# Kernel optimization log

Measured on AMD Instinct MI355X. Metric: run time of the kernel, lower is better.

The kernel has to match this reference:

```python
import jax, jax.numpy as jnp
import numpy as np
import math

D_MODEL = 1024
N_HEADS = 16
D_FF = 4096
KERNEL = 25
EPS = 1e-5


def setup_inputs() -> dict:
    key = jax.random.key(0)
    ks = jax.random.split(key, 16)
    B, L, D = 2, 2048, D_MODEL
    s = 0.02
    inp = {
        'x': jax.random.normal(ks[0], (B, L, D), dtype=jnp.float32),
        'Wq': jax.random.normal(ks[1], (D, D), dtype=jnp.float32) * s,
        'bq': jnp.zeros((D,), jnp.float32),
        'Wk': jax.random.normal(ks[2], (D, D), dtype=jnp.float32) * s,
        'bk': jnp.zeros((D,), jnp.float32),
        'Wv': jax.random.normal(ks[3], (D, D), dtype=jnp.float32) * s,
        'bv': jnp.zeros((D,), jnp.float32),
        'Wo': jax.random.normal(ks[4], (D, D), dtype=jnp.float32) * s,
        'bo': jnp.zeros((D,), jnp.float32),
        'W1': jax.random.normal(ks[5], (D_FF, D), dtype=jnp.float32) * s,
        'b1': jnp.zeros((D_FF,), jnp.float32),
        'W2': jax.random.normal(ks[6], (D, D_FF), dtype=jnp.float32) * s,
        'b2': jnp.zeros((D,), jnp.float32),
        'g1': jnp.ones((D,), jnp.float32),
        'be1': jnp.zeros((D,), jnp.float32),
        'g2': jnp.ones((D,), jnp.float32),
        'be2': jnp.zeros((D,), jnp.float32),
    }
    return inp


def moving_avg(x):
    # torch AvgPool1d(kernel=25, stride=1, padding=12, count_include_pad=True)
    # x: (B, L, D) -> trend: (B, L, D)
    pad = KERNEL // 2
    xp = jnp.pad(x, ((0, 0), (pad, pad), (0, 0)))
    c = jnp.cumsum(xp, axis=1)
    c = jnp.concatenate([jnp.zeros_like(c[:, :1]), c], axis=1)
    return (c[:, KERNEL:] - c[:, :-KERNEL]) / KERNEL


def layernorm(x, g, b):
    mu = jnp.mean(x, axis=-1, keepdims=True)
    var = jnp.mean((x - mu) ** 2, axis=-1, keepdims=True)
    return (x - mu) * jax.lax.rsqrt(var + EPS) * g + b


def reference(x, Wq, bq, Wk, bk, Wv, bv, Wo, bo, W1, b1, W2, b2, g1, be1, g2, be2):
    B, L, D = x.shape
    H, dk = N_HEADS, D // N_HEADS
    # projections (torch Linear: y = x @ W.T + b)
    q = (x @ Wq.T + bq).reshape(B, L, H, dk).transpose(0, 2, 1, 3)
    k = (x @ Wk.T + bk).reshape(B, L, H, dk).transpose(0, 2, 1, 3)
    v = (x @ Wv.T + bv).reshape(B, L, H, dk).transpose(0, 2, 1, 3)
    scores = jnp.einsum('bhld,bhmd->bhlm', q, k) / math.sqrt(dk)
    t = jnp.arange(L, dtype=jnp.float32)
    time_bias = -0.1 * jnp.abs(t[None, :] - t[:, None])  # (L, L)
    attn = jax.nn.softmax(scores + time_bias[None, None], axis=-1)
    ao = jnp.einsum('bhlm,bhmd->bhld', attn, v)
    ao = ao.transpose(0, 2, 1, 3).reshape(B, L, D)
    attn_out = ao @ Wo.T + bo
    x = x + attn_out
    x = moving_avg(x)  # trend kept (x, _ = decomp1(x))
    x = layernorm(x, g1, be1)
    ff = jax.nn.gelu(x @ W1.T + b1, approximate=False) @ W2.T + b2
    x = x + ff
    x = moving_avg(x)  # trend kept again
    x = layernorm(x, g2, be2)
    return x
```

## Files before the change

### kernel.cpp

```cpp
#include <hip/hip_runtime.h>
#include <hip/hip_bf16.h>
#include <math.h>

#define DMODEL 1024
#define LSEQ   2048
#define BATCH  2
#define NHEADS 16
#define DHEAD  64
#define DFF    4096
#define MROWS  (BATCH*LSEQ)

typedef __attribute__((ext_vector_type(8))) short short8;
typedef __attribute__((ext_vector_type(4))) float f32x4;
using bf16 = __hip_bfloat16;

static __device__ __forceinline__ f32x4 mfma16(short8 a, short8 b, f32x4 c) {
    return __builtin_amdgcn_mfma_f32_16x16x32_bf16(a, b, c, 0, 0, 0);
}

static __device__ __forceinline__ void gload16(const void* g, void* l) {
    __builtin_amdgcn_global_load_lds(
        (const __attribute__((address_space(1))) char*)g,
        (__attribute__((address_space(3))) char*)l, 16, 0, 0);
}

static __device__ __forceinline__ bf16 b16(float v) { return __float2bfloat16(v); }
static __device__ __forceinline__ float f32(bf16 v) { return __bfloat162float(v); }

__global__ void f2b_all(const float* __restrict__ x, const float* __restrict__ W1,
                        const float* __restrict__ W2,
                        const float* Wq, const float* Wk, const float* Wv, const float* Wo,
                        const float* bq, const float* bk, const float* bv,
                        bf16* __restrict__ xb, bf16* __restrict__ W1b, bf16* __restrict__ W2b,
                        bf16* __restrict__ Wqkvb, bf16* __restrict__ Wob,
                        float* __restrict__ bqkv) {
    int i = blockIdx.x * blockDim.x + threadIdx.x;
    const float* in; bf16* out;
    switch (blockIdx.y) {
        case 0: in = x;  out = xb;  break;
        case 1: in = W1; out = W1b; break;
        case 2: in = W2; out = W2b; break;
        case 3: {
            const int w = i >> 18, r = i & ((1 << 18) - 1);
            const float* ws4[4] = {Wq, Wk, Wv, Wo};
            bf16* os4[4] = {Wqkvb, Wqkvb + (DMODEL * DMODEL), Wqkvb + 2 * (DMODEL * DMODEL), Wob};
            float4 v = reinterpret_cast<const float4*>(ws4[w])[r];
            union { ushort4 u; bf16 h[4]; } o;
            o.h[0] = b16(v.x); o.h[1] = b16(v.y); o.h[2] = b16(v.z); o.h[3] = b16(v.w);
            reinterpret_cast<ushort4*>(os4[w])[r] = o.u;
            return;
        }
        default:
            if (i < DMODEL / 4) {
                reinterpret_cast<float4*>(bqkv)[i]                  = reinterpret_cast<const float4*>(bq)[i];
                reinterpret_cast<float4*>(bqkv)[DMODEL / 4 + i]     = reinterpret_cast<const float4*>(bk)[i];
                reinterpret_cast<float4*>(bqkv)[2 * DMODEL / 4 + i] = reinterpret_cast<const float4*>(bv)[i];
            }
            return;
    }
    float4 v = reinterpret_cast<const float4*>(in)[i];
    union { ushort4 u; bf16 h[4]; } o;
    o.h[0] = b16(v.x); o.h[1] = b16(v.y); o.h[2] = b16(v.z); o.h[3] = b16(v.w);
    reinterpret_cast<ushort4*>(out)[i] = o.u;
}

template<int S, bool RESB16>
__global__ __launch_bounds__(256) void reduce_kernel(const void* __restrict__ resv,
                                                     const bf16* __restrict__ P,
                                                     const float* __restrict__ bias,
                                                     bf16* __restrict__ outb, int n4) {
    int i = blockIdx.x * blockDim.x + threadIdx.x;
    if (i >= n4) return;
    float4 acc;
    if (RESB16) {
        union { ushort4 u; bf16 h[4]; } r;
        r.u = reinterpret_cast<const ushort4*>(resv)[i];
        acc.x = f32(r.h[0]); acc.y = f32(r.h[1]); acc.z = f32(r.h[2]); acc.w = f32(r.h[3]);
    } else {
        acc = reinterpret_cast<const float4*>(resv)[i];
    }
#pragma unroll
    for (int s = 0; s < S; ++s) {
        union { ushort4 u; bf16 h[4]; } p;
        p.u = reinterpret_cast<const ushort4*>(P)[i + (size_t)s * (MROWS * DMODEL / 4)];
        acc.x += f32(p.h[0]); acc.y += f32(p.h[1]);
        acc.z += f32(p.h[2]); acc.w += f32(p.h[3]);
    }
    float4 bs = reinterpret_cast<const float4*>(bias)[i & (DMODEL / 4 - 1)];
    union { ushort4 u; bf16 h[4]; } o;
    o.h[0] = b16(acc.x + bs.x); o.h[1] = b16(acc.y + bs.y);
    o.h[2] = b16(acc.z + bs.z); o.h[3] = b16(acc.w + bs.w);
    reinterpret_cast<ushort4*>(outb)[i] = o.u;
}

template<int EPI>
__global__ __launch_bounds__(512, 2) void gemm256(const bf16* __restrict__ A,
                                                  const bf16* __restrict__ W,
                                                  const float* __restrict__ bias,
                                                  void* __restrict__ Cout,
                                                  int M, int N, int lda, int ldw,
                                                  int K, int nn) {
    __shared__ bf16 sm[49152];
    const int t    = threadIdx.x;
    const int wave = t >> 6, lane = t & 63;
    const int lr   = lane & 15, lkb = lane >> 4;
    const int wm   = wave >> 2, wn = wave & 3;
    const int sk   = blockIdx.z;

    const int nwg = gridDim.x;
    const int bid = blockIdx.x;
    const int wg  = (bid & 7) * (nwg >> 3) + (bid >> 3);
    const int m0  = (wg / nn) * 256;
    const int n0  = (wg % nn) * 256;

    const bf16* src[4];
    int dbase[4];
#pragma unroll
    for (int u = 0; u < 4; ++u) {
        const int q  = t + (u & 1) * 512;
        const int R  = q >> 3;
        const int ss = (q & 7) ^ (R & 7);
        const int rp = ss >> 2, c = (ss & 3) * 8;
        if (u < 2) src[u] = A + (size_t)(m0 + 2 * R + rp) * lda + (size_t)sk * K + c;
        else       src[u] = W + (size_t)(n0 + 2 * R + rp) * ldw + (size_t)sk * K + c;
        dbase[u] = ((u >> 1) ? 16384 : 0) + (wave * 64 + (u & 1) * 512) * 16;
    }
    char* smb = (char*)sm;

    int aoff[8], boff[4];
#pragma unroll
    for (int i = 0; i < 8; ++i) {
        const int r = wm * 128 + i * 16 + lr, R = r >> 1;
        aoff[i] = R * 128 + ((((r & 1) << 2) | lkb) ^ (R & 7)) * 16;
    }
#pragma unroll
    for (int j = 0; j < 4; ++j) {
        const int r = wn * 64 + j * 16 + lr, R = r >> 1;
        boff[j] = 16384 + R * 128 + ((((r & 1) << 2) | lkb) ^ (R & 7)) * 16;
    }

    f32x4 acc[8][4];
#pragma unroll
    for (int i = 0; i < 8; ++i)
#pragma unroll
        for (int j = 0; j < 4; ++j)
            acc[i][j] = (f32x4){0.f, 0.f, 0.f, 0.f};

    const int nt = K >> 5;
    auto STAGE = [&](int bufoff, int kt) {
        const int koff = kt * 32;
#pragma unroll
        for (int u = 0; u < 4; ++u)
            gload16(src[u] + koff, smb + bufoff + dbase[u]);
    };
    auto STAGE2 = [&](int bufoff, int kt, int u0) {
        const int koff = kt * 32;
        gload16(src[u0] + koff, smb + bufoff + dbase[u0]);
        gload16(src[u0 + 1] + koff, smb + bufoff + dbase[u0 + 1]);
    };

    STAGE(0, 0);
    if (nt > 1) STAGE(32768, 1);
    __builtin_amdgcn_sched_barrier(0);
    if (nt > 1) asm volatile("s_waitcnt vmcnt(4)" ::: "memory");
    else        asm volatile("s_waitcnt vmcnt(0)" ::: "memory");
    __builtin_amdgcn_s_barrier();
    __builtin_amdgcn_sched_barrier(0);

    int curoff = 0, stgoff = 65536;
    for (int kt = 0; kt < nt; ++kt) {
        const bool pre = (kt + 2 < nt);
        short8 b0, b1, b2, b3, x0, x1;

        b0 = *reinterpret_cast<const short8*>(smb + curoff + boff[0]);
        b1 = *reinterpret_cast<const short8*>(smb + curoff + boff[1]);
        b2 = *reinterpret_cast<const short8*>(smb + curoff + boff[2]);
        b3 = *reinterpret_cast<const short8*>(smb + curoff + boff[3]);
        x0 = *reinterpret_cast<const short8*>(smb + curoff + aoff[0]);
        x1 = *reinterpret_cast<const short8*>(smb + curoff + aoff[1]);
        if (pre) STAGE2(stgoff, kt + 2, 0);
        __builtin_amdgcn_sched_barrier(0);
        __builtin_amdgcn_s_barrier();
        asm volatile("s_waitcnt lgkmcnt(0)" ::: "memory");
        __builtin_amdgcn_sched_barrier(0);
        __builtin_amdgcn_s_setprio(1);
        acc[0][0] = mfma16(b0, x0, acc[0][0]); acc[0][1] = mfma16(b1, x0, acc[0][1]);
        acc[0][2] = mfma16(b2, x0, acc[0][2]); acc[0][3] = mfma16(b3, x0, acc[0][3]);
        acc[1][0] = mfma16(b0, x1, acc[1][0]); acc[1][1] = mfma16(b1, x1, acc[1][1]);
        acc[1][2] = mfma16(b2, x1, acc[1][2]); acc[1][3] = mfma16(b3, x1, acc[1][3]);
        __builtin_amdgcn_s_setprio(0);

        x0 = *reinterpret_cast<const short8*>(smb + curoff + aoff[2]);
        x1 = *reinterpret_cast<const short8*>(smb + curoff + aoff[3]);
        if (pre) STAGE2(stgoff, kt + 2, 2);
        __builtin_amdgcn_sched_barrier(0);
        __builtin_amdgcn_s_barrier();
        asm volatile("s_waitcnt lgkmcnt(0)" ::: "memory");
        __builtin_amdgcn_sched_barrier(0);
        __builtin_amdgcn_s_setprio(1);
        acc[2][0] = mfma16(b0, x0, acc[2][0]); acc[2][1] = mfma16(b1, x0, acc[2][1]);
        acc[2][2] = mfma16(b2, x0, acc[2][2]); acc[2][3] = mfma16(b3, x0, acc[2][3]);
        acc[3][0] = mfma16(b0, x1, acc[3][0]); acc[3][1] = mfma16(b1, x1, acc[3][1]);
        acc[3][2] = mfma16(b2, x1, acc[3][2]); acc[3][3] = mfma16(b3, x1, acc[3][3]);
        __builtin_amdgcn_s_setprio(0);

        x0 = *reinterpret_cast<const short8*>(smb + curoff + aoff[4]);
        x1 = *reinterpret_cast<const short8*>(smb + curoff + aoff[5]);
        __builtin_amdgcn_sched_barrier(0);
        __builtin_amdgcn_s_barrier();
        asm volatile("s_waitcnt lgkmcnt(0)" ::: "memory");
        __builtin_amdgcn_sched_barrier(0);
        __builtin_amdgcn_s_setprio(1);
        acc[4][0] = mfma16(b0, x0, acc[4][0]); acc[4][1] = mfma16(b1, x0, acc[4][1]);
        acc[4][2] = mfma16(b2, x0, acc[4][2]); acc[4][3] = mfma16(b3, x0, acc[4][3]);
        acc[5][0] = mfma16(b0, x1, acc[5][0]); acc[5][1] = mfma16(b1, x1, acc[5][1]);
        acc[5][2] = mfma16(b2, x1, acc[5][2]); acc[5][3] = mfma16(b3, x1, acc[5][3]);
        __builtin_amdgcn_s_setprio(0);

        x0 = *reinterpret_cast<const short8*>(smb + curoff + aoff[6]);
        x1 = *reinterpret_cast<const short8*>(smb + curoff + aoff[7]);
        __builtin_amdgcn_sched_barrier(0);
        __builtin_amdgcn_s_barrier();
        asm volatile("s_waitcnt lgkmcnt(0)" ::: "memory");
        __builtin_amdgcn_sched_barrier(0);
        __builtin_amdgcn_s_setprio(1);
        acc[6][0] = mfma16(b0, x0, acc[6][0]); acc[6][1] = mfma16(b1, x0, acc[6][1]);
        acc[6][2] = mfma16(b2, x0, acc[6][2]); acc[6][3] = mfma16(b3, x0, acc[6][3]);
        acc[7][0] = mfma16(b0, x1, acc[7][0]); acc[7][1] = mfma16(b1, x1, acc[7][1]);
        acc[7][2] = mfma16(b2, x1, acc[7][2]); acc[7][3] = mfma16(b3, x1, acc[7][3]);
        __builtin_amdgcn_s_setprio(0);
        if (kt + 1 < nt) {
            __builtin_amdgcn_sched_barrier(0);
            if (pre) asm volatile("s_waitcnt vmcnt(4)" ::: "memory");
            else     asm volatile("s_waitcnt vmcnt(0)" ::: "memory");
            __builtin_amdgcn_s_barrier();
            __builtin_amdgcn_sched_barrier(0);
        }
        if (pre) stgoff = (stgoff == 65536) ? 0 : stgoff + 32768;
        curoff = (curoff == 65536) ? 0 : curoff + 32768;
    }

#pragma unroll
    for (int i = 0; i < 8; ++i) {
        const int row = m0 + wm * 128 + i * 16 + lr;
#pragma unroll
        for (int j = 0; j < 4; ++j) {
            const int col = n0 + wn * 64 + j * 16 + lkb * 4;
            f32x4 v = acc[i][j];
            if (EPI != 3) {
                float4 bs = *reinterpret_cast<const float4*>(&bias[col]);
                v[0] += bs.x; v[1] += bs.y; v[2] += bs.z; v[3] += bs.w;
            }
            if (EPI == 0) {
                float4 ov; ov.x = v[0]; ov.y = v[1]; ov.z = v[2]; ov.w = v[3];
                *reinterpret_cast<float4*>(&((float*)Cout)[(size_t)row * N + col]) = ov;
            } else if (EPI == 1) {
                union { ushort4 u; bf16 h[4]; } ob;
#pragma unroll
                for (int q = 0; q < 4; ++q) {
                    float x = v[q];
                    float u2 = x * (1.5957691216f + 0.0713548162f * x * x);
                    float e = __expf(fminf(u2, 60.f));
                    ob.h[q] = b16(x * (e / (e + 1.f)));
                }
                *reinterpret_cast<ushort4*>(
                    &reinterpret_cast<bf16*>(Cout)[(size_t)row * N + col]) = ob.u;
            } else if (EPI == 2) {
                union { ushort4 u; bf16 h[4]; } ob;
#pragma unroll
                for (int q = 0; q < 4; ++q) ob.h[q] = b16(v[q]);
                *reinterpret_cast<ushort4*>(
                    &reinterpret_cast<bf16*>(Cout)[(size_t)row * N + col]) = ob.u;
            } else {
                bf16* Pp = (bf16*)Cout + (size_t)sk * M * N;
                union { ushort4 u; bf16 h[4]; } ob;
#pragma unroll
                for (int q = 0; q < 4; ++q) ob.h[q] = b16(v[q]);
                *reinterpret_cast<ushort4*>(&Pp[(size_t)row * N + col]) = ob.u;
            }
        }
    }
}

__global__ __launch_bounds__(256) void attn_kernel(const bf16* __restrict__ Q,
                                                   const bf16* __restrict__ Km,
                                                   const bf16* __restrict__ V,
                                                   bf16* __restrict__ O,
                                                   int ldq, int ldo) {
    __shared__ bf16 Qs[64][72];
    __shared__ bf16 Ks[64][72];
    __shared__ bf16 VsT[64][72];
    __shared__ bf16 Ps[64][72];
    const int t    = threadIdx.x;
    const int wave = t >> 6, lane = t & 63;
    const int lr   = lane & 15, lkb = lane >> 4;
    const int qt   = blockIdx.x;
    const int q0   = qt * 64;
    const int b    = blockIdx.y >> 4, h = blockIdx.y & 15;
    const size_t base  = (size_t)b * LSEQ * ldq + (size_t)h * DHEAD;
    const size_t baseo = (size_t)b * LSEQ * ldo + (size_t)h * DHEAD;

#pragma unroll
    for (int p = 0; p < 2; ++p) {
        int idx = t + p * 256;
        int row = idx >> 3, c = (idx & 7) * 8;
        *reinterpret_cast<uint4*>(&Qs[row][c]) =
            *reinterpret_cast<const uint4*>(&Q[base + (size_t)(q0 + row) * ldq + c]);
    }
    __syncthreads();
    short8 qa[2];
    qa[0] = *reinterpret_cast<const short8*>(&Qs[wave * 16 + lr][lkb * 8]);
    qa[1] = *reinterpret_cast<const short8*>(&Qs[wave * 16 + lr][32 + lkb * 8]);

    f32x4 o[4];
#pragma unroll
    for (int dj = 0; dj < 4; ++dj) o[dj] = (f32x4){0.f, 0.f, 0.f, 0.f};
    float mrun[4], lrun[4];
#pragma unroll
    for (int q = 0; q < 4; ++q) { mrun[q] = -1e30f; lrun[q] = 0.f; }

    int kt0 = qt - 1; if (kt0 < 0) kt0 = 0;
    int kt1 = qt + 1; if (kt1 > LSEQ / 64 - 1) kt1 = LSEQ / 64 - 1;

    for (int kt = kt0; kt <= kt1; ++kt) {
        const int k0 = kt * 64;
        __syncthreads();
#pragma unroll
        for (int p = 0; p < 2; ++p) {
            int idx = t + p * 256;
            int row = idx >> 3, c = (idx & 7) * 8;
            *reinterpret_cast<uint4*>(&Ks[row][c]) =
                *reinterpret_cast<const uint4*>(&Km[base + (size_t)(k0 + row) * ldq + c]);
        }
        {
            const int vl = lane, vw = wave;
#pragma unroll
            for (int p = 0; p < 2; ++p) {
                int c = vw * 8 + p * 32;
                union { uint4 u; bf16 hh[8]; } tv;
                tv.u = *reinterpret_cast<const uint4*>(&V[base + (size_t)(k0 + vl) * ldq + c]);
#pragma unroll
                for (int e = 0; e < 8; ++e) VsT[c + e][vl] = tv.hh[e];
            }
        }
        __syncthreads();

        f32x4 s[4];
#pragma unroll
        for (int j = 0; j < 4; ++j) {
            short8 kb0 = *reinterpret_cast<const short8*>(&Ks[j * 16 + lr][lkb * 8]);
            short8 kb1 = *reinterpret_cast<const short8*>(&Ks[j * 16 + lr][32 + lkb * 8]);
            f32x4 z = (f32x4){0.f, 0.f, 0.f, 0.f};
            z = mfma16(qa[0], kb0, z);
            z = mfma16(qa[1], kb1, z);
            s[j] = z;
        }
        float mx[4];
#pragma unroll
        for (int q = 0; q < 4; ++q) mx[q] = -1e30f;
#pragma unroll
        for (int j = 0; j < 4; ++j) {
            int cm = k0 + j * 16 + lr;
#pragma unroll
            for (int q = 0; q < 4; ++q) {
                int rq = q0 + wave * 16 + lkb * 4 + q;
                float sv = s[j][q] * 0.125f - 0.1f * fabsf((float)(rq - cm));
                s[j][q] = sv;
                mx[q] = fmaxf(mx[q], sv);
            }
        }
#pragma unroll
        for (int q = 0; q < 4; ++q) {
#pragma unroll
            for (int off = 1; off < 16; off <<= 1)
                mx[q] = fmaxf(mx[q], __shfl_xor(mx[q], off));
        }
        float alpha[4];
#pragma unroll
        for (int q = 0; q < 4; ++q) {
            float mnew = fmaxf(mrun[q], mx[q]);
            alpha[q] = __expf(mrun[q] - mnew);
            mrun[q] = mnew;
        }
        float rs[4] = {0.f, 0.f, 0.f, 0.f};
#pragma unroll
        for (int j = 0; j < 4; ++j) {
#pragma unroll
            for (int q = 0; q < 4; ++q) {
                float p = __expf(s[j][q] - mrun[q]);
                rs[q] += p;
                Ps[wave * 16 + lkb * 4 + q][j * 16 + lr] = b16(p);
            }
        }
#pragma unroll
        for (int q = 0; q < 4; ++q) {
#pragma unroll
            for (int off = 1; off < 16; off <<= 1)
                rs[q] += __shfl_xor(rs[q], off);
            lrun[q] = lrun[q] * alpha[q] + rs[q];
        }
#pragma unroll
        for (int dj = 0; dj < 4; ++dj)
#pragma unroll
            for (int q = 0; q < 4; ++q) o[dj][q] *= alpha[q];

        short8 pa0 = *reinterpret_cast<const short8*>(&Ps[wave * 16 + lr][lkb * 8]);
        short8 pa1 = *reinterpret_cast<const short8*>(&Ps[wave * 16 + lr][32 + lkb * 8]);
#pragma unroll
        for (int dj = 0; dj < 4; ++dj) {
            short8 vb0 = *reinterpret_cast<const short8*>(&VsT[dj * 16 + lr][lkb * 8]);
            short8 vb1 = *reinterpret_cast<const short8*>(&VsT[dj * 16 + lr][32 + lkb * 8]);
            o[dj] = mfma16(pa0, vb0, o[dj]);
            o[dj] = mfma16(pa1, vb1, o[dj]);
        }
    }

#pragma unroll
    for (int dj = 0; dj < 4; ++dj) {
#pragma unroll
        for (int q = 0; q < 4; ++q) {
            int row = q0 + wave * 16 + lkb * 4 + q;
            int col = dj * 16 + lr;
            float val = o[dj][q] / lrun[q];
            O[baseo + (size_t)row * ldo + col] = b16(val);
        }
    }
}

__global__ __launch_bounds__(256) void mavg_ln4_kernel(const bf16* __restrict__ r,
                                                       const float* __restrict__ g,
                                                       const float* __restrict__ be,
                                                       float* __restrict__ out,
                                                       bf16* __restrict__ outb) {
    const int gid = (blockIdx.x & 7) * (MROWS / 8 / 4) + (blockIdx.x >> 3);
    const int row0 = gid * 4;
    const int b = row0 >> 11, l0 = row0 & 2047;
    const int t = threadIdx.x, c = t * 4;
    const bf16* base = r + (size_t)b * LSEQ * DMODEL;

    float4 s[4];
#pragma unroll
    for (int o = 0; o < 4; ++o) s[o] = (float4){0.f, 0.f, 0.f, 0.f};
    int j0 = l0 - 12; if (j0 < 0) j0 = 0;
    int j1 = l0 + 15; if (j1 > LSEQ - 1) j1 = LSEQ - 1;
    for (int j = j0; j <= j1; ++j) {
        union { ushort4 u; bf16 h[4]; } rv;
        rv.u = *reinterpret_cast<const ushort4*>(&base[(size_t)j * DMODEL + c]);
        float4 v; v.x = f32(rv.h[0]); v.y = f32(rv.h[1]); v.z = f32(rv.h[2]); v.w = f32(rv.h[3]);
#pragma unroll
        for (int o = 0; o < 4; ++o) {
            const int lo = l0 + o;
            if (j >= lo - 12 && j <= lo + 12) {
                s[o].x += v.x; s[o].y += v.y; s[o].z += v.z; s[o].w += v.w;
            }
        }
    }
    const float kinv = 1.0f / 25.0f;
    float4 tr[4];
    float p1[4], p2[4];
#pragma unroll
    for (int o = 0; o < 4; ++o) {
        tr[o].x = s[o].x * kinv; tr[o].y = s[o].y * kinv;
        tr[o].z = s[o].z * kinv; tr[o].w = s[o].w * kinv;
        p1[o] = tr[o].x + tr[o].y + tr[o].z + tr[o].w;
        p2[o] = tr[o].x * tr[o].x + tr[o].y * tr[o].y + tr[o].z * tr[o].z + tr[o].w * tr[o].w;
    }
    const int lane = t & 63, wv = t >> 6;
#pragma unroll
    for (int off = 1; off < 64; off <<= 1) {
#pragma unroll
        for (int o = 0; o < 4; ++o) {
            p1[o] += __shfl_xor(p1[o], off);
            p2[o] += __shfl_xor(p2[o], off);
        }
    }
    __shared__ float red[4][8];
    if (lane == 0) {
#pragma unroll
        for (int o = 0; o < 4; ++o) { red[wv][o] = p1[o]; red[wv][4 + o] = p2[o]; }
    }
    __syncthreads();
    float4 gg = *reinterpret_cast<const float4*>(&g[c]);
    float4 bb = *reinterpret_cast<const float4*>(&be[c]);
#pragma unroll
    for (int o = 0; o < 4; ++o) {
        float q1 = red[0][o] + red[1][o] + red[2][o] + red[3][o];
        float q2 = red[0][4 + o] + red[1][4 + o] + red[2][4 + o] + red[3][4 + o];
        const float mu  = q1 * (1.0f / 1024.0f);
        const float var = q2 * (1.0f / 1024.0f) - mu * mu;
        const float inv = rsqrtf(var + 1e-5f);
        float o0 = (tr[o].x - mu) * inv * gg.x + bb.x;
        float o1 = (tr[o].y - mu) * inv * gg.y + bb.y;
        float o2 = (tr[o].z - mu) * inv * gg.z + bb.z;
        float o3 = (tr[o].w - mu) * inv * gg.w + bb.w;
        if (out) {
            float4 ov; ov.x = o0; ov.y = o1; ov.z = o2; ov.w = o3;
            *reinterpret_cast<float4*>(&out[(size_t)(row0 + o) * DMODEL + c]) = ov;
        }
        if (outb) {
            union { ushort4 u; bf16 hh[4]; } ob;
            ob.hh[0] = b16(o0); ob.hh[1] = b16(o1); ob.hh[2] = b16(o2); ob.hh[3] = b16(o3);
            reinterpret_cast<ushort4*>(outb + (size_t)(row0 + o) * DMODEL)[t] = ob.u;
        }
    }
}

extern "C" void kernel_launch(void* const* d_in, const int* in_sizes, int n_in,
                              void* d_out, int out_size, void* d_ws, size_t ws_size,
                              hipStream_t stream) {
    const float* x   = (const float*)d_in[0];
    const float* Wq  = (const float*)d_in[1];
    const float* bq  = (const float*)d_in[2];
    const float* Wk  = (const float*)d_in[3];
    const float* bk  = (const float*)d_in[4];
    const float* Wv  = (const float*)d_in[5];
    const float* bv  = (const float*)d_in[6];
    const float* Wo  = (const float*)d_in[7];
    const float* bo  = (const float*)d_in[8];
    const float* W1  = (const float*)d_in[9];
    const float* b1  = (const float*)d_in[10];
    const float* W2  = (const float*)d_in[11];
    const float* b2  = (const float*)d_in[12];
    const float* g1  = (const float*)d_in[13];
    const float* be1 = (const float*)d_in[14];
    const float* g2  = (const float*)d_in[15];
    const float* be2 = (const float*)d_in[16];
    float* out = (float*)d_out;
    char* ws = (char*)d_ws;
    const size_t MB = 1u << 20;

    bf16* xb    = (bf16*)(ws + 0);
    bf16* rrb   = (bf16*)(ws + 8 * MB);
    bf16* qkvb  = (bf16*)(ws + 16 * MB);
    bf16* ab    = (bf16*)(ws + 16 * MB);
    bf16* hb    = (bf16*)(ws + 24 * MB);
    bf16* aob   = (bf16*)(ws + 40 * MB);
    bf16* Wqkvb = (bf16*)(ws + 48 * MB);
    bf16* Wob   = (bf16*)(ws + 54 * MB);
    bf16* W1b   = (bf16*)(ws + 56 * MB);
    bf16* W2b   = (bf16*)(ws + 64 * MB);
    bf16* P     = (bf16*)(ws + 72 * MB);
    float* bqkv = (float*)(ws + 136 * MB);

    f2b_all<<<dim3((MROWS * DMODEL / 4) / 256, 5), 256, 0, stream>>>(
        x, W1, W2, Wq, Wk, Wv, Wo, bq, bk, bv,
        xb, W1b, W2b, Wqkvb, Wob, bqkv);

    gemm256<2><<<dim3(192, 1, 1), 512, 0, stream>>>(xb, Wqkvb, bqkv, qkvb,
                                                    MROWS, 3 * DMODEL, DMODEL, DMODEL, DMODEL, 12);
    attn_kernel<<<dim3(32, 32), 256, 0, stream>>>(qkvb, qkvb + DMODEL, qkvb + 2 * DMODEL,
                                                  aob, 3 * DMODEL, DMODEL);
    gemm256<3><<<dim3(64, 1, 4), 512, 0, stream>>>(aob, Wob, nullptr, P,
                                                   MROWS, DMODEL, DMODEL, DMODEL, DMODEL / 4, 4);
    reduce_kernel<4, false><<<(MROWS * DMODEL / 4) / 256, 256, 0, stream>>>(
        x, P, bo, rrb, MROWS * DMODEL / 4);
    mavg_ln4_kernel<<<MROWS / 4, 256, 0, stream>>>(rrb, g1, be1, nullptr, ab);
    gemm256<1><<<dim3(256, 1, 1), 512, 0, stream>>>(ab, W1b, b1, hb,
                                                    MROWS, DFF, DMODEL, DMODEL, DMODEL, 16);
    gemm256<3><<<dim3(64, 1, 4), 512, 0, stream>>>(hb, W2b, nullptr, P,
                                                   MROWS, DMODEL, DFF, DFF, DFF / 4, 4);
    reduce_kernel<4, true><<<(MROWS * DMODEL / 4) / 256, 256, 0, stream>>>(
        ab, P, b2, rrb, MROWS * DMODEL / 4);
    mavg_ln4_kernel<<<MROWS / 4, 256, 0, stream>>>(rrb, g2, be2, out, nullptr);
}
```

Measured before the change: 240.1 us.

## Replace 256x256 GEMM with 256x128 tile, 4-wave double-buffered kernel

The 512-thread 256x256 GEMM with a triple-buffered, barrier-interleaved pipeline is replaced by a 256-thread kernel computing 256x128 tiles. Each wave still owns a 128x64 sub-tile, and K tiles are double-buffered: the next tile is staged, then all fragments are loaded and a full 32-MFMA block is issued. Grids double to expose more workgroups, and the Wo projection drops from split-K 4 to split-K 2 with a matching reduce. In exchange, each K step now has only one tile of prefetch lookahead and a full vmcnt(0) wait plus barrier, so memory latency may be less hidden, and A-tile reuse per workgroup is halved.

New measurement: 236.3 us. No clear change (-1.6%).

```diff
diff --git a/kernel.cpp b/kernel.cpp
--- a/kernel.cpp
+++ b/kernel.cpp
@@ -94,36 +94,40 @@
 }
 
 template<int EPI>
-__global__ __launch_bounds__(512, 2) void gemm256(const bf16* __restrict__ A,
-                                                  const bf16* __restrict__ W,
-                                                  const float* __restrict__ bias,
-                                                  void* __restrict__ Cout,
-                                                  int M, int N, int lda, int ldw,
-                                                  int K, int nn) {
-    __shared__ bf16 sm[49152];
+__global__ __launch_bounds__(256, 2) void gemmT(const bf16* __restrict__ A,
+                                                const bf16* __restrict__ W,
+                                                const float* __restrict__ bias,
+                                                void* __restrict__ Cout,
+                                                int M, int N, int lda, int ldw,
+                                                int K, int nn) {
+    __shared__ bf16 sm[24576];
     const int t    = threadIdx.x;
     const int wave = t >> 6, lane = t & 63;
     const int lr   = lane & 15, lkb = lane >> 4;
-    const int wm   = wave >> 2, wn = wave & 3;
+    const int wm   = wave >> 1, wn = wave & 1;
     const int sk   = blockIdx.z;
 
     const int nwg = gridDim.x;
     const int bid = blockIdx.x;
     const int wg  = (bid & 7) * (nwg >> 3) + (bid >> 3);
     const int m0  = (wg / nn) * 256;
-    const int n0  = (wg % nn) * 256;
-
-    const bf16* src[4];
-    int dbase[4];
-#pragma unroll
-    for (int u = 0; u < 4; ++u) {
-        const int q  = t + (u & 1) * 512;
+    const int n0  = (wg % nn) * 128;
+
+    const bf16* src[6];
+    int dbase[6];
+#pragma unroll
+    for (int u = 0; u < 6; ++u) {
+        const int q  = (u < 4 ? u : u - 4) * 256 + t;
         const int R  = q >> 3;
         const int ss = (q & 7) ^ (R & 7);
         const int rp = ss >> 2, c = (ss & 3) * 8;
-        if (u < 2) src[u] = A + (size_t)(m0 + 2 * R + rp) * lda + (size_t)sk * K + c;
-        else       src[u] = W + (size_t)(n0 + 2 * R + rp) * ldw + (size_t)sk * K + c;
-        dbase[u] = ((u >> 1) ? 16384 : 0) + (wave * 64 + (u & 1) * 512) * 16;
+        if (u < 4) {
+            src[u]   = A + (size_t)(m0 + 2 * R + rp) * lda + (size_t)sk * K + c;
+            dbase[u] = u * 4096 + wave * 1024;
+        } else {
+            src[u]   = W + (size_t)(n0 + 2 * R + rp) * ldw + (size_t)sk * K + c;
+            dbase[u] = 16384 + (u - 4) * 4096 + wave * 1024;
+        }
     }
     char* smb = (char*)sm;
 
@@ -150,94 +154,38 @@
     auto STAGE = [&](int bufoff, int kt) {
         const int koff = kt * 32;
 #pragma unroll
-        for (int u = 0; u < 4; ++u)
+        for (int u = 0; u < 6; ++u)
             gload16(src[u] + koff, smb + bufoff + dbase[u]);
     };
-    auto STAGE2 = [&](int bufoff, int kt, int u0) {
-        const int koff = kt * 32;
-        gload16(src[u0] + koff, smb + bufoff + dbase[u0]);
-        gload16(src[u0 + 1] + koff, smb + bufoff + dbase[u0 + 1]);
-    };
 
     STAGE(0, 0);
-    if (nt > 1) STAGE(32768, 1);
     __builtin_amdgcn_sched_barrier(0);
-    if (nt > 1) asm volatile("s_waitcnt vmcnt(4)" ::: "memory");
-    else        asm volatile("s_waitcnt vmcnt(0)" ::: "memory");
+    asm volatile("s_waitcnt vmcnt(0)" ::: "memory");
     __builtin_amdgcn_s_barrier();
     __builtin_amdgcn_sched_barrier(0);
 
-    int curoff = 0, stgoff = 65536;
+    int cur = 0;
     for (int kt = 0; kt < nt; ++kt) {
-        const bool pre = (kt + 2 < nt);
-        short8 b0, b1, b2, b3, x0, x1;
-
-        b0 = *reinterpret_cast<const short8*>(smb + curoff + boff[0]);
-        b1 = *reinterpret_cast<const short8*>(smb + curoff + boff[1]);
-        b2 = *reinterpret_cast<const short8*>(smb + curoff + boff[2]);
-        b3 = *reinterpret_cast<const short8*>(smb + curoff + boff[3]);
-        x0 = *reinterpret_cast<const short8*>(smb + curoff + aoff[0]);
-        x1 = *reinterpret_cast<const short8*>(smb + curoff + aoff[1]);
-        if (pre) STAGE2(stgoff, kt + 2, 0);
+        if (kt + 1 < nt) STAGE((cur ^ 1) * 24576, kt + 1);
+        short8 a[8], b[4];
+#pragma unroll
+        for (int i = 0; i < 8; ++i)
+            a[i] = *reinterpret_cast<const short8*>(smb + cur * 24576 + aoff[i]);
+#pragma unroll
+        for (int j = 0; j < 4; ++j)
+            b[j] = *reinterpret_cast<const short8*>(smb + cur * 24576 + boff[j]);
+        __builtin_amdgcn_s_setprio(1);
+#pragma unroll
+        for (int i = 0; i < 8; ++i)
+#pragma unroll
+            for (int j = 0; j < 4; ++j)
+                acc[i][j] = mfma16(b[j], a[i], acc[i][j]);
+        __builtin_amdgcn_s_setprio(0);
         __builtin_amdgcn_sched_barrier(0);
+        asm volatile("s_waitcnt vmcnt(0)" ::: "memory");
         __builtin_amdgcn_s_barrier();
-        asm volatile("s_waitcnt lgkmcnt(0)" ::: "memory");
         __builtin_amdgcn_sched_barrier(0);
-        __builtin_amdgcn_s_setprio(1);
-        acc[0][0] = mfma16(b0, x0, acc[0][0]); acc[0][1] = mfma16(b1, x0, acc[0][1]);
-        acc[0][2] = mfma16(b2, x0, acc[0][2]); acc[0][3] = mfma16(b3, x0, acc[0][3]);
-        acc[1][0] = mfma16(b0, x1, acc[1][0]); acc[1][1] = mfma16(b1, x1, acc[1][1]);
-        acc[1][2] = mfma16(b2, x1, acc[1][2]); acc[1][3] = mfma16(b3, x1, acc[1][3]);
-        __builtin_amdgcn_s_setprio(0);
-
-        x0 = *reinterpret_cast<const short8*>(smb + curoff + aoff[2]);
-        x1 = *reinterpret_cast<const short8*>(smb + curoff + aoff[3]);
-        if (pre) STAGE2(stgoff, kt + 2, 2);
-        __builtin_amdgcn_sched_barrier(0);
-        __builtin_amdgcn_s_barrier();
-        asm volatile("s_waitcnt lgkmcnt(0)" ::: "memory");
-        __builtin_amdgcn_sched_barrier(0);
-        __builtin_amdgcn_s_setprio(1);
-        acc[2][0] = mfma16(b0, x0, acc[2][0]); acc[2][1] = mfma16(b1, x0, acc[2][1]);
-        acc[2][2] = mfma16(b2, x0, acc[2][2]); acc[2][3] = mfma16(b3, x0, acc[2][3]);
-        acc[3][0] = mfma16(b0, x1, acc[3][0]); acc[3][1] = mfma16(b1, x1, acc[3][1]);
-        acc[3][2] = mfma16(b2, x1, acc[3][2]); acc[3][3] = mfma16(b3, x1, acc[3][3]);
-        __builtin_amdgcn_s_setprio(0);
-
-        x0 = *reinterpret_cast<const short8*>(smb + curoff + aoff[4]);
-        x1 = *reinterpret_cast<const short8*>(smb + curoff + aoff[5]);
-        __builtin_amdgcn_sched_barrier(0);
-        __builtin_amdgcn_s_barrier();
-        asm volatile("s_waitcnt lgkmcnt(0)" ::: "memory");
-        __builtin_amdgcn_sched_barrier(0);
-        __builtin_amdgcn_s_setprio(1);
-        acc[4][0] = mfma16(b0, x0, acc[4][0]); acc[4][1] = mfma16(b1, x0, acc[4][1]);
-        acc[4][2] = mfma16(b2, x0, acc[4][2]); acc[4][3] = mfma16(b3, x0, acc[4][3]);
-        acc[5][0] = mfma16(b0, x1, acc[5][0]); acc[5][1] = mfma16(b1, x1, acc[5][1]);
-        acc[5][2] = mfma16(b2, x1, acc[5][2]); acc[5][3] = mfma16(b3, x1, acc[5][3]);
-        __builtin_amdgcn_s_setprio(0);
-
-        x0 = *reinterpret_cast<const short8*>(smb + curoff + aoff[6]);
-        x1 = *reinterpret_cast<const short8*>(smb + curoff + aoff[7]);
-        __builtin_amdgcn_sched_barrier(0);
-        __builtin_amdgcn_s_barrier();
-        asm volatile("s_waitcnt lgkmcnt(0)" ::: "memory");
-        __builtin_amdgcn_sched_barrier(0);
-        __builtin_amdgcn_s_setprio(1);
-        acc[6][0] = mfma16(b0, x0, acc[6][0]); acc[6][1] = mfma16(b1, x0, acc[6][1]);
-        acc[6][2] = mfma16(b2, x0, acc[6][2]); acc[6][3] = mfma16(b3, x0, acc[6][3]);
-        acc[7][0] = mfma16(b0, x1, acc[7][0]); acc[7][1] = mfma16(b1, x1, acc[7][1]);
-        acc[7][2] = mfma16(b2, x1, acc[7][2]); acc[7][3] = mfma16(b3, x1, acc[7][3]);
-        __builtin_amdgcn_s_setprio(0);
-        if (kt + 1 < nt) {
-            __builtin_amdgcn_sched_barrier(0);
-            if (pre) asm volatile("s_waitcnt vmcnt(4)" ::: "memory");
-            else     asm volatile("s_waitcnt vmcnt(0)" ::: "memory");
-            __builtin_amdgcn_s_barrier();
-            __builtin_amdgcn_sched_barrier(0);
-        }
-        if (pre) stgoff = (stgoff == 65536) ? 0 : stgoff + 32768;
-        curoff = (curoff == 65536) ? 0 : curoff + 32768;
+        cur ^= 1;
     }
 
 #pragma unroll
@@ -546,19 +494,19 @@
         x, W1, W2, Wq, Wk, Wv, Wo, bq, bk, bv,
         xb, W1b, W2b, Wqkvb, Wob, bqkv);
 
-    gemm256<2><<<dim3(192, 1, 1), 512, 0, stream>>>(xb, Wqkvb, bqkv, qkvb,
-                                                    MROWS, 3 * DMODEL, DMODEL, DMODEL, DMODEL, 12);
+    gemmT<2><<<dim3(384, 1, 1), 256, 0, stream>>>(xb, Wqkvb, bqkv, qkvb,
+                                                  MROWS, 3 * DMODEL, DMODEL, DMODEL, DMODEL, 24);
     attn_kernel<<<dim3(32, 32), 256, 0, stream>>>(qkvb, qkvb + DMODEL, qkvb + 2 * DMODEL,
                                                   aob, 3 * DMODEL, DMODEL);
-    gemm256<3><<<dim3(64, 1, 4), 512, 0, stream>>>(aob, Wob, nullptr, P,
-                                                   MROWS, DMODEL, DMODEL, DMODEL, DMODEL / 4, 4);
-    reduce_kernel<4, false><<<(MROWS * DMODEL / 4) / 256, 256, 0, stream>>>(
+    gemmT<3><<<dim3(128, 1, 2), 256, 0, stream>>>(aob, Wob, nullptr, P,
+                                                  MROWS, DMODEL, DMODEL, DMODEL, DMODEL / 2, 8);
+    reduce_kernel<2, false><<<(MROWS * DMODEL / 4) / 256, 256, 0, stream>>>(
         x, P, bo, rrb, MROWS * DMODEL / 4);
     mavg_ln4_kernel<<<MROWS / 4, 256, 0, stream>>>(rrb, g1, be1, nullptr, ab);
-    gemm256<1><<<dim3(256, 1, 1), 512, 0, stream>>>(ab, W1b, b1, hb,
-                                                    MROWS, DFF, DMODEL, DMODEL, DMODEL, 16);
-    gemm256<3><<<dim3(64, 1, 4), 512, 0, stream>>>(hb, W2b, nullptr, P,
-                                                   MROWS, DMODEL, DFF, DFF, DFF / 4, 4);
+    gemmT<1><<<dim3(512, 1, 1), 256, 0, stream>>>(ab, W1b, b1, hb,
+                                                  MROWS, DFF, DMODEL, DMODEL, DMODEL, 32);
+    gemmT<3><<<dim3(128, 1, 4), 256, 0, stream>>>(hb, W2b, nullptr, P,
+                                                  MROWS, DMODEL, DFF, DFF, DFF / 4, 8);
     reduce_kernel<4, true><<<(MROWS * DMODEL / 4) / 256, 256, 0, stream>>>(
         ab, P, b2, rrb, MROWS * DMODEL / 4);
     mavg_ln4_kernel<<<MROWS / 4, 256, 0, stream>>>(rrb, g2, be2, out, nullptr);
```
